# Optimization experiments

Measured on AMD Instinct MI355X. Metric: run time of the kernel, lower is better.

Reference implementation:

```python
import jax, jax.numpy as jnp
import numpy as np
from jax import lax

EPS = 1e-5  # torch BatchNorm2d default eps


def _binconv(x, w, b):
    # BinarizeConv2d: sign-binarize input and weight, dense conv, then add bias
    y = lax.conv_general_dilated(jnp.sign(x), jnp.sign(w), (2, 2), [(1, 1), (1, 1)],
                                 dimension_numbers=('NCHW', 'OIHW', 'NCHW'))
    return y + b[None, :, None, None]


def _bn(x, g, be):
    # BatchNorm2d in training mode: biased batch statistics over (N,H,W)
    m = jnp.mean(x, axis=(0, 2, 3), keepdims=True)
    v = jnp.mean((x - m) ** 2, axis=(0, 2, 3), keepdims=True)
    return (x - m) * (g[None, :, None, None] / jnp.sqrt(v + EPS)) + be[None, :, None, None]


def setup_inputs() -> dict:
    key = jax.random.key(0)
    ks = jax.random.split(key, 20)
    B = 8192
    d = {"x": jax.random.normal(ks[0], (B, 6, 32, 48), jnp.float32)}
    chans = [(12, 6), (24, 12), (48, 24), (96, 48)]
    i = 1
    for n, (co, ci) in enumerate(chans, 1):
        d[f"w{n}"] = jax.random.normal(ks[i], (co, ci, 5, 5), jnp.float32) * 0.1; i += 1
        d[f"b{n}"] = jax.random.normal(ks[i], (co,), jnp.float32) * 0.01; i += 1
        d[f"g{n}"] = jnp.ones((co,), jnp.float32)
        d[f"be{n}"] = jnp.zeros((co,), jnp.float32)
    d["wl"] = jax.random.normal(ks[i], (360, 192), jnp.float32) * 0.1; i += 1
    d["bl"] = jax.random.normal(ks[i], (360,), jnp.float32) * 0.01
    return d


def reference(x, w1, b1, g1, be1, w2, b2, g2, be2, w3, b3, g3, be3,
              w4, b4, g4, be4, wl, bl):
    x1 = jnp.clip(_bn(_binconv(x, w1, b1), g1, be1), 0.0, 1.0)
    x2 = jnp.clip(_bn(_binconv(x1, w2, b2), g2, be2), 0.0, 1.0)
    x3 = jnp.clip(_bn(_binconv(x2, w3, b3), g3, be3), 0.0, 1.0)
    x4 = jnp.clip(_bn(_binconv(x3, w4, b4), g4, be4), 0.0, 1.0)
    x4 = x4.reshape(-1, 192)  # (B, 96*1*2)
    # BinarizeLinear: in_features=192 != 784 so input is binarized too
    return jnp.sign(x4) @ jnp.sign(wl).T + bl
```

## Files before the change

### kernel.cpp

```cpp
#include <hip/hip_runtime.h>
#include <stdint.h>

typedef unsigned long long u64;
typedef uint32_t u32;
typedef uint16_t u16;

#define NIMG 8192

static const size_t O_TOT = 0;
static const size_t O_X1  = 4096;
static const size_t O_A2  = O_X1 + (size_t)NIMG*32*50*2;
static const size_t O_A3  = O_A2 + (size_t)NIMG*15*25*2;
static const size_t O_A4  = O_A3 + (size_t)NIMG*7*13*4;
static const size_t O_W1  = O_A4 + (size_t)NIMG*3*7*8;
static const size_t O_W2  = O_W1 + 120*8;
static const size_t O_W3  = O_W2 + 240*8;
static const size_t O_W4  = O_W3 + 960*8;
static const size_t O_WL  = O_W4 + 3840*8;
static const size_t O_S   = O_WL + 2160*8;

__global__ __launch_bounds__(256) void binx_k(const float* __restrict__ x,
                         const float* w1, const float* w2, const float* w3,
                         const float* w4, const float* wl,
                         u16* __restrict__ X1,
                         u64* W1, u64* W2, u64* W3, u64* W4, u64* WL, u64* tot) {
  if (blockIdx.x >= 49152) {
    int b = blockIdx.x - 49152;
    int t = threadIdx.x;
    if (b == 5) { tot[t] = 0; tot[t+256] = 0; return; }
    int u = b*256 + t;
    if (u < 60) {
      int co = u/5, kh = u%5;
      u64 wp=0, wn=0;
      for (int kw=0; kw<5; kw++) for (int ci=0; ci<6; ci++) {
        float v = w1[co*150 + ci*25 + kh*5 + kw];
        int pos = 6*kw + ci;
        if (v > 0.f) wp |= 1ull<<pos; else if (v < 0.f) wn |= 1ull<<pos;
      }
      W1[u*2]   = wp | (wn<<32);
      W1[u*2+1] = wn | (wp<<32);
    } else if (u < 180) {
      int q = u-60; int co=q/5, kh=q%5;
      u64 wp=0, wn=0;
      for (int kw=0; kw<5; kw++) for (int ci=0; ci<12; ci++) {
        float v = w2[co*300 + ci*25 + kh*5 + kw];
        int pos = 12*kw+ci;
        if (v>0.f) wp |= 1ull<<pos; else if (v<0.f) wn |= 1ull<<pos;
      }
      W2[q*2] = wp; W2[q*2+1] = wn;
    } else if (u < 420) {
      int q = u-180; int co=q/5, kh=q%5;
      u64 wp[2]={0,0}, wn[2]={0,0};
      for (int kw=0; kw<5; kw++) for (int ci=0; ci<24; ci++) {
        float v = w3[co*600 + ci*25 + kh*5 + kw];
        int pos = 24*kw+ci;
        if (v>0.f) wp[pos>>6] |= 1ull<<(pos&63); else if (v<0.f) wn[pos>>6] |= 1ull<<(pos&63);
      }
      W3[q*4]=wp[0]; W3[q*4+1]=wp[1]; W3[q*4+2]=wn[0]; W3[q*4+3]=wn[1];
    } else if (u < 900) {
      int q = u-420; int co=q/5, kh=q%5;
      u64 wp[4]={0,0,0,0}, wn[4]={0,0,0,0};
      for (int kw=0; kw<5; kw++) for (int ci=0; ci<48; ci++) {
        float v = w4[co*1200 + ci*25 + kh*5 + kw];
        int pos = 48*kw+ci;
        if (v>0.f) wp[pos>>6] |= 1ull<<(pos&63); else if (v<0.f) wn[pos>>6] |= 1ull<<(pos&63);
      }
      for (int j=0;j<4;j++){ W4[q*8+j]=wp[j]; W4[q*8+4+j]=wn[j]; }
    } else if (u < 1260) {
      int o = u-900;
      u64 wp[3]={0,0,0}, wn[3]={0,0,0};
      for (int k=0;k<192;k++){
        float v = wl[o*192+k];
        if (v>0.f) wp[k>>6] |= 1ull<<(k&63); else if (v<0.f) wn[k>>6] |= 1ull<<(k&63);
      }
      for (int j=0;j<3;j++){ WL[o*6+j]=wp[j]; WL[o*6+3+j]=wn[j]; }
    }
    return;
  }
  int gid = blockIdx.x*256+threadIdx.x;
  int n = gid / 1536, r = gid % 1536, h = r/48, w = r%48;
  const float* xp = x + (size_t)n*9216 + h*48 + w;
  u32 v = 0;
  #pragma unroll
  for (int c=0;c<6;c++){ float t = xp[c*1536];
    v |= (t>0.f ? 1u:0u)<<c; v |= (t<0.f ? 1u:0u)<<(8+c); }
  u16* row = X1 + (size_t)n*1600 + h*50;
  row[w+1] = (u16)v;
  if (w==0)  row[0]  = 0;
  if (w==47) row[49] = 0;
}

#define LSTR 265
template<int NR>
__device__ long long tree_reduce(const int (&vals)[NR], int* lds){
  int t = threadIdx.x;
  #pragma unroll
  for (int r=0;r<NR;r++) lds[r*LSTR + t] = vals[r];
  __syncthreads();
  if (t < NR*8) {
    int r = t % NR, seg = t / NR;
    const int* row = lds + r*LSTR + seg*32;
    int s = 0;
    #pragma unroll
    for (int i=0;i<32;i++) s += row[i];
    lds[r*LSTR + 256 + seg] = s;
  }
  __syncthreads();
  long long res = 0;
  if (t < NR) {
    const int* row = lds + t*LSTR + 256;
    int s = 0;
    #pragma unroll
    for (int i=0;i<8;i++) s += row[i];
    res = s;
  }
  __syncthreads();
  return res;
}

__global__ __launch_bounds__(256) void conv1_k(const u16* __restrict__ X1, const u64* __restrict__ W1,
                                               u32* __restrict__ S1) {
  int pix = blockIdx.x*256+threadIdx.x;
  int n = pix/345, r = pix%345, oh = r/23, ow = r%23;
  int S[12];
  #pragma unroll
  for (int i=0;i<12;i++) S[i]=0;
  const u16* base = X1 + (size_t)n*1600;
  for (int kh=0; kh<5; kh++){
    int row = 2*oh-1+kh;
    if ((unsigned)row >= 32u) continue;
    const u16* p = base + row*50 + 2*ow;
    u64 xp=0, xn=0;
    #pragma unroll
    for (int i=0;i<5;i++){ u32 v = p[i];
      xp |= (u64)(v & 63u) << (6*i);
      xn |= (u64)(v >> 8)  << (6*i); }
    u64 X = xp | (xn<<32);
    const u64* wr = W1 + kh*2;
    #pragma unroll
    for (int co=0;co<12;co++)
      S[co] += __popcll(X & wr[co*10]) - __popcll(X & wr[co*10+1]);
  }
  u32* o = S1 + (size_t)pix*3;
  #pragma unroll
  for (int j=0;j<3;j++)
    o[j] = (u32)(S[4*j]&255) | ((u32)(S[4*j+1]&255)<<8) |
           ((u32)(S[4*j+2]&255)<<16) | ((u32)(S[4*j+3]&255)<<24);
}

__global__ __launch_bounds__(256) void stats1_k(const u32* __restrict__ S1, u64* __restrict__ tot){
  __shared__ int lds[24*LSTR];
  int acc[12], q[12];
  #pragma unroll
  for (int i=0;i<12;i++){ acc[i]=0; q[i]=0; }
  int nt = gridDim.x*256;
  for (int p = blockIdx.x*256+threadIdx.x; p < NIMG*345; p += nt){
    u32 w0=S1[(size_t)p*3], w1=S1[(size_t)p*3+1], w2=S1[(size_t)p*3+2];
    #pragma unroll
    for (int c=0;c<12;c++){
      u32 w = (c<4)?w0:(c<8)?w1:w2;
      int v = (int)(w << ((3-(c&3))*8)) >> 24;
      acc[c]+=v; q[c]+=v*v;
    }
  }
  int vals[24];
  #pragma unroll
  for (int c=0;c<12;c++){ vals[c]=acc[c]; vals[12+c]=q[c]; }
  long long rs = tree_reduce<24>(vals, lds);
  int t = threadIdx.x;
  if (t < 12)       atomicAdd(&tot[t*2],        (u64)rs);
  else if (t < 24)  atomicAdd(&tot[(t-12)*2+1], (u64)rs);
}

__global__ __launch_bounds__(256) void conv2_k(const u16* __restrict__ A2, const u64* __restrict__ W2,
                                               short* __restrict__ S2, u64* __restrict__ tot) {
  __shared__ int lds[24*LSTR];
  int pix = blockIdx.x*256+threadIdx.x;
  int n = pix/77, r = pix%77, oh = r/11, ow = r%11;
  int S[24];
  #pragma unroll
  for (int i=0;i<24;i++) S[i]=0;
  const u16* base = A2 + (size_t)n*375;
  for (int kh=0; kh<5; kh++){
    int row = 2*oh-1+kh;
    if ((unsigned)row >= 15u) continue;
    const u16* p = base + row*25 + 2*ow;
    u64 X=0;
    #pragma unroll
    for (int i=0;i<5;i++) X |= (u64)p[i] << (12*i);
    const u64* wr = W2 + kh*2;
    #pragma unroll
    for (int co=0;co<24;co++)
      S[co] += __popcll(X & wr[co*10]) - __popcll(X & wr[co*10+1]);
  }
  short* o = S2 + (size_t)pix*24;
  #pragma unroll
  for (int co=0;co<24;co++) o[co] = (short)S[co];
  long long rs = tree_reduce<24>(S, lds);
  int t = threadIdx.x;
  if (t < 24) atomicAdd(&tot[t*2], (u64)rs);
  int q[24];
  #pragma unroll
  for (int c=0;c<24;c++) q[c]=S[c]*S[c];
  rs = tree_reduce<24>(q, lds);
  if (t < 24) atomicAdd(&tot[t*2+1], (u64)rs);
}

__global__ __launch_bounds__(256) void conv3_k(const u32* __restrict__ A3, const u64* __restrict__ W3,
                                               short* __restrict__ S3, u64* __restrict__ tot) {
  __shared__ int lds[24*LSTR];
  int pix = blockIdx.x*256+threadIdx.x;
  int n = pix/15, r = pix%15, oh = r/5, ow = r%5;
  int S[48];
  #pragma unroll
  for (int i=0;i<48;i++) S[i]=0;
  const u32* base = A3 + (size_t)n*91;
  for (int kh=0; kh<5; kh++){
    int row = 2*oh-1+kh;
    if ((unsigned)row >= 7u) continue;
    const u32* p = base + row*13 + 2*ow;
    u64 a0=p[0],a1=p[1],a2=p[2],a3=p[3],a4=p[4];
    u64 x0 = a0 | (a1<<24) | (a2<<48);
    u64 x1 = (a2>>16) | (a3<<8) | (a4<<32);
    const u64* wr = W3 + kh*4;
    #pragma unroll
    for (int co=0;co<48;co++){
      const u64* q = wr + co*20;
      S[co] += __popcll(x0 & q[0]) + __popcll(x1 & q[1])
             - __popcll(x0 & q[2]) - __popcll(x1 & q[3]);
    }
  }
  short* o = S3 + (size_t)pix*48;
  #pragma unroll
  for (int co=0;co<48;co++) o[co] = (short)S[co];
  int t = threadIdx.x;
  for (int c0=0; c0<48; c0+=24){
    int v[24];
    #pragma unroll
    for (int j=0;j<24;j++) v[j]=S[c0+j];
    long long rs = tree_reduce<24>(v, lds);
    if (t < 24) atomicAdd(&tot[(c0+t)*2], (u64)rs);
    #pragma unroll
    for (int j=0;j<24;j++) v[j]=S[c0+j]*S[c0+j];
    rs = tree_reduce<24>(v, lds);
    if (t < 24) atomicAdd(&tot[(c0+t)*2+1], (u64)rs);
  }
}

__global__ __launch_bounds__(256) void conv4_k(const u64* __restrict__ A4, const u64* __restrict__ W4,
                                               short* __restrict__ S4, u64* __restrict__ tot) {
  __shared__ int l4[96*66];
  int gid = blockIdx.x*256+threadIdx.x;
  int pix = gid>>2, grp = gid&3;
  int n = pix>>1, ow = pix&1;
  int S[24];
  #pragma unroll
  for (int i=0;i<24;i++) S[i]=0;
  const u64* base = A4 + (size_t)n*21;
  for (int kh=0; kh<5; kh++){
    int row = kh-1;
    if ((unsigned)row >= 3u) continue;
    const u64* p = base + row*7 + 2*ow;
    u64 a0=p[0],a1=p[1],a2=p[2],a3=p[3],a4=p[4];
    u64 x0 = a0 | (a1<<48);
    u64 x1 = (a1>>16) | (a2<<32);
    u64 x2 = (a2>>32) | (a3<<16);
    u64 x3 = a4;
    const u64* wr = W4 + kh*8;
    #pragma unroll
    for (int j=0;j<24;j++){
      const u64* q = wr + (grp*24+j)*40;
      S[j] += __popcll(x0&q[0]) + __popcll(x1&q[1]) + __popcll(x2&q[2]) + __popcll(x3&q[3])
            - __popcll(x0&q[4]) - __popcll(x1&q[5]) - __popcll(x2&q[6]) - __popcll(x3&q[7]);
    }
  }
  short* o = S4 + (size_t)pix*96 + grp*24;
  #pragma unroll
  for (int j=0;j<24;j++) o[j] = (short)S[j];
  int t = threadIdx.x, col = t>>2;
  #pragma unroll
  for (int j=0;j<24;j++) l4[(grp*24+j)*66 + col] = S[j];
  __syncthreads();
  if (t < 96){
    int s=0; const int* row = l4 + t*66;
    #pragma unroll
    for (int i=0;i<64;i++) s += row[i];
    atomicAdd(&tot[t*2], (u64)(long long)s);
  }
  __syncthreads();
  #pragma unroll
  for (int j=0;j<24;j++) l4[(grp*24+j)*66 + col] = S[j]*S[j];
  __syncthreads();
  if (t < 96){
    int s=0; const int* row = l4 + t*66;
    #pragma unroll
    for (int i=0;i<64;i++) s += row[i];
    atomicAdd(&tot[t*2+1], (u64)(long long)s);
  }
}

template<int C>
__device__ void bn_params(const u64* tot, const float* g, const float* be, double cnt,
                          float* s_mu, float* s_k, float* s_be) {
  int t = threadIdx.x;
  if (t < C) {
    long long sum = (long long)tot[t*2];
    long long sq  = (long long)tot[t*2+1];
    double mu  = (double)sum / cnt;
    double var = (double)sq / cnt - mu*mu;
    double kk  = (double)g[t] / sqrt(var + 1e-5);
    s_mu[t] = (float)mu; s_k[t] = (float)kk; s_be[t] = be[t];
  }
  __syncthreads();
}

__global__ __launch_bounds__(256) void thresh1_k(const u32* __restrict__ S1, const u64* tot,
                                                 const float* g, const float* be, u16* __restrict__ A2){
  __shared__ float mu[12], kk[12], bb[12];
  bn_params<12>(tot, g, be, 2826240.0, mu, kk, bb);
  int pix = blockIdx.x*256+threadIdx.x;
  int n=pix/345, r=pix%345, oh=r/23, ow=r%23;
  const u32* s = S1 + (size_t)pix*3;
  u32 w0=s[0], w1=s[1], w2=s[2];
  u32 wv=0;
  #pragma unroll
  for (int c=0;c<12;c++){
    u32 w = (c<4) ? w0 : (c<8) ? w1 : w2;
    int sv = (int)(w << ((3-(c&3))*8)) >> 24;
    float v = ((float)sv-mu[c])*kk[c]+bb[c];
    wv |= (v>0.f?1u:0u)<<c;
  }
  u16* row = A2 + (size_t)n*375 + oh*25;
  row[ow+1] = (u16)wv;
  if (ow==0)  row[0]  = 0;
  if (ow==22) row[24] = 0;
}

__global__ __launch_bounds__(256) void thresh2_k(const short* __restrict__ S2, const u64* tot,
                                                 const float* g, const float* be, u32* __restrict__ A3){
  __shared__ float mu[24], kk[24], bb[24];
  bn_params<24>(tot, g, be, 630784.0, mu, kk, bb);
  int pix = blockIdx.x*256+threadIdx.x;
  int n=pix/77, r=pix%77, oh=r/11, ow=r%11;
  const short* s = S2 + (size_t)pix*24;
  u32 wv=0;
  #pragma unroll
  for (int c=0;c<24;c++){ float v = ((float)s[c]-mu[c])*kk[c]+bb[c]; wv |= (v>0.f?1u:0u)<<c; }
  u32* row = A3 + (size_t)n*91 + oh*13;
  row[ow+1] = wv;
  if (ow==0)  row[0]  = 0;
  if (ow==10) row[12] = 0;
}

__global__ __launch_bounds__(256) void thresh3_k(const short* __restrict__ S3, const u64* tot,
                                                 const float* g, const float* be, u64* __restrict__ A4){
  __shared__ float mu[48], kk[48], bb[48];
  bn_params<48>(tot, g, be, 122880.0, mu, kk, bb);
  int pix = blockIdx.x*256+threadIdx.x;
  int n=pix/15, r=pix%15, oh=r/5, ow=r%5;
  const short* s = S3 + (size_t)pix*48;
  u64 wv=0;
  #pragma unroll
  for (int c=0;c<48;c++){ float v = ((float)s[c]-mu[c])*kk[c]+bb[c]; wv |= (u64)(v>0.f?1u:0u)<<c; }
  u64* row = A4 + (size_t)n*21 + oh*7;
  row[ow+1] = wv;
  if (ow==0) row[0] = 0;
  if (ow==4) row[6] = 0;
}

__global__ __launch_bounds__(256) void lin4_k(const short* __restrict__ S4, const u64* tot,
                                              const float* g, const float* be,
                                              const u64* __restrict__ WL, const float* __restrict__ bl,
                                              float* __restrict__ out){
  __shared__ float mu[96], kk[96], bb[96];
  __shared__ u64 aLs[64*3];
  __shared__ u64 wls[2160];
  bn_params<96>(tot, g, be, 16384.0, mu, kk, bb);
  int t = threadIdx.x;
  for (int i=t; i<2160; i+=256) wls[i] = WL[i];
  if (t < 64){
    int n = blockIdx.x*64 + t;
    u64 a[3]={0,0,0};
    for (int w=0;w<2;w++){
      const short* s = S4 + ((size_t)n*2+w)*96;
      #pragma unroll
      for (int c=0;c<96;c++){
        float v = ((float)s[c]-mu[c])*kk[c]+bb[c];
        int k = c*2+w;
        if (v>0.f) a[k>>6] |= 1ull<<(k&63);
      }
    }
    aLs[t*3]=a[0]; aLs[t*3+1]=a[1]; aLs[t*3+2]=a[2];
  }
  __syncthreads();
  float* ob = out + (size_t)blockIdx.x*23040;
  #pragma unroll 2
  for (int i=0;i<90;i++){
    int li = i*256+t;
    int nl = li/360, o = li%360;
    const u64* a = &aLs[nl*3];
    const u64* w = &wls[o*6];
    int S = __popcll(a[0]&w[0]) + __popcll(a[1]&w[1]) + __popcll(a[2]&w[2])
          - __popcll(a[0]&w[3]) - __popcll(a[1]&w[4]) - __popcll(a[2]&w[5]);
    ob[li] = (float)S + bl[o];
  }
}

extern "C" void kernel_launch(void* const* d_in, const int* in_sizes, int n_in,
                              void* d_out, int out_size, void* d_ws, size_t ws_size,
                              hipStream_t stream) {
  const float* x  = (const float*)d_in[0];
  const float* w1 = (const float*)d_in[1];
  const float* g1 = (const float*)d_in[3];
  const float* be1= (const float*)d_in[4];
  const float* w2 = (const float*)d_in[5];
  const float* g2 = (const float*)d_in[7];
  const float* be2= (const float*)d_in[8];
  const float* w3 = (const float*)d_in[9];
  const float* g3 = (const float*)d_in[11];
  const float* be3= (const float*)d_in[12];
  const float* w4 = (const float*)d_in[13];
  const float* g4 = (const float*)d_in[15];
  const float* be4= (const float*)d_in[16];
  const float* wl = (const float*)d_in[17];
  const float* bl = (const float*)d_in[18];

  char* ws = (char*)d_ws;
  u64* tot = (u64*)(ws + O_TOT);
  u16* X1  = (u16*)(ws + O_X1);
  u16* A2  = (u16*)(ws + O_A2);
  u32* A3  = (u32*)(ws + O_A3);
  u64* A4  = (u64*)(ws + O_A4);
  u64* W1  = (u64*)(ws + O_W1);
  u64* W2  = (u64*)(ws + O_W2);
  u64* W3  = (u64*)(ws + O_W3);
  u64* W4  = (u64*)(ws + O_W4);
  u64* WL  = (u64*)(ws + O_WL);
  u32*   S1b = (u32*)(ws + O_S);
  short* Sb  = (short*)(ws + O_S);

  binx_k<<<49158,256,0,stream>>>(x, w1,w2,w3,w4,wl, X1, W1,W2,W3,W4,WL, tot);

  conv1_k<<<11040,256,0,stream>>>(X1, W1, S1b);
  stats1_k<<<1024,256,0,stream>>>(S1b, tot+0);
  thresh1_k<<<11040,256,0,stream>>>(S1b, tot+0, g1, be1, A2);

  conv2_k<<<2464,256,0,stream>>>(A2, W2, Sb, tot+24);
  thresh2_k<<<2464,256,0,stream>>>(Sb, tot+24, g2, be2, A3);

  conv3_k<<<480,256,0,stream>>>(A3, W3, Sb, tot+72);
  thresh3_k<<<480,256,0,stream>>>(Sb, tot+72, g3, be3, A4);

  conv4_k<<<256,256,0,stream>>>(A4, W4, Sb, tot+168);
  lin4_k<<<128,256,0,stream>>>(Sb, tot+168, g4, be4, WL, bl, (float*)d_out);
}
```

Measured before the change: 882.2 us.

## Fuse input binarization into conv1 with per-image shared-memory bit image

Merges the input sign-binarization kernel and the first binary convolution into one kernel with one block per image. Each block loads its image with float4 reads, packs the sign bits into a shared-memory bitplane using atomicOr, and computes the W1 weight bits in shared memory. The conv1 popcount loop then reads that shared bitplane directly, so the X1 global intermediate and one launch go away. The costs are shared-memory atomics, 345 pixels spread over 256 threads (a second, mostly idle pass), and every block recomputing the W1 bits.

```diff
diff --git a/kernel.cpp b/kernel.cpp
--- a/kernel.cpp
+++ b/kernel.cpp
@@ -8,38 +8,26 @@
 #define NIMG 8192
 
 static const size_t O_TOT = 0;
-static const size_t O_X1  = 4096;
-static const size_t O_A2  = O_X1 + (size_t)NIMG*32*50*2;
+static const size_t O_A2  = 4096;
 static const size_t O_A3  = O_A2 + (size_t)NIMG*15*25*2;
 static const size_t O_A4  = O_A3 + (size_t)NIMG*7*13*4;
-static const size_t O_W1  = O_A4 + (size_t)NIMG*3*7*8;
-static const size_t O_W2  = O_W1 + 120*8;
+static const size_t O_W2  = O_A4 + (size_t)NIMG*3*7*8;
 static const size_t O_W3  = O_W2 + 240*8;
 static const size_t O_W4  = O_W3 + 960*8;
 static const size_t O_WL  = O_W4 + 3840*8;
 static const size_t O_S   = O_WL + 2160*8;
 
-__global__ __launch_bounds__(256) void binx_k(const float* __restrict__ x,
+__global__ __launch_bounds__(256) void bc1_k(const float* __restrict__ x,
                          const float* w1, const float* w2, const float* w3,
                          const float* w4, const float* wl,
-                         u16* __restrict__ X1,
-                         u64* W1, u64* W2, u64* W3, u64* W4, u64* WL, u64* tot) {
-  if (blockIdx.x >= 49152) {
-    int b = blockIdx.x - 49152;
+                         u64* W2, u64* W3, u64* W4, u64* WL, u64* tot,
+                         u32* __restrict__ S1) {
+  if (blockIdx.x >= NIMG) {
+    int b = blockIdx.x - NIMG;
     int t = threadIdx.x;
     if (b == 5) { tot[t] = 0; tot[t+256] = 0; return; }
     int u = b*256 + t;
-    if (u < 60) {
-      int co = u/5, kh = u%5;
-      u64 wp=0, wn=0;
-      for (int kw=0; kw<5; kw++) for (int ci=0; ci<6; ci++) {
-        float v = w1[co*150 + ci*25 + kh*5 + kw];
-        int pos = 6*kw + ci;
-        if (v > 0.f) wp |= 1ull<<pos; else if (v < 0.f) wn |= 1ull<<pos;
-      }
-      W1[u*2]   = wp | (wn<<32);
-      W1[u*2+1] = wn | (wp<<32);
-    } else if (u < 180) {
+    if (u >= 60 && u < 180) {
       int q = u-60; int co=q/5, kh=q%5;
       u64 wp=0, wn=0;
       for (int kw=0; kw<5; kw++) for (int ci=0; ci<12; ci++) {
@@ -48,7 +36,7 @@
         if (v>0.f) wp |= 1ull<<pos; else if (v<0.f) wn |= 1ull<<pos;
       }
       W2[q*2] = wp; W2[q*2+1] = wn;
-    } else if (u < 420) {
+    } else if (u >= 180 && u < 420) {
       int q = u-180; int co=q/5, kh=q%5;
       u64 wp[2]={0,0}, wn[2]={0,0};
       for (int kw=0; kw<5; kw++) for (int ci=0; ci<24; ci++) {
@@ -57,7 +45,7 @@
         if (v>0.f) wp[pos>>6] |= 1ull<<(pos&63); else if (v<0.f) wn[pos>>6] |= 1ull<<(pos&63);
       }
       W3[q*4]=wp[0]; W3[q*4+1]=wp[1]; W3[q*4+2]=wn[0]; W3[q*4+3]=wn[1];
-    } else if (u < 900) {
+    } else if (u >= 420 && u < 900) {
       int q = u-420; int co=q/5, kh=q%5;
       u64 wp[4]={0,0,0,0}, wn[4]={0,0,0,0};
       for (int kw=0; kw<5; kw++) for (int ci=0; ci<48; ci++) {
@@ -66,7 +54,7 @@
         if (v>0.f) wp[pos>>6] |= 1ull<<(pos&63); else if (v<0.f) wn[pos>>6] |= 1ull<<(pos&63);
       }
       for (int j=0;j<4;j++){ W4[q*8+j]=wp[j]; W4[q*8+4+j]=wn[j]; }
-    } else if (u < 1260) {
+    } else if (u >= 900 && u < 1260) {
       int o = u-900;
       u64 wp[3]={0,0,0}, wn[3]={0,0,0};
       for (int k=0;k<192;k++){
@@ -77,17 +65,71 @@
     }
     return;
   }
-  int gid = blockIdx.x*256+threadIdx.x;
-  int n = gid / 1536, r = gid % 1536, h = r/48, w = r%48;
-  const float* xp = x + (size_t)n*9216 + h*48 + w;
-  u32 v = 0;
-  #pragma unroll
-  for (int c=0;c<6;c++){ float t = xp[c*1536];
-    v |= (t>0.f ? 1u:0u)<<c; v |= (t<0.f ? 1u:0u)<<(8+c); }
-  u16* row = X1 + (size_t)n*1600 + h*50;
-  row[w+1] = (u16)v;
-  if (w==0)  row[0]  = 0;
-  if (w==47) row[49] = 0;
+
+  __shared__ u32 img[32*26];
+  __shared__ u64 W1s[120];
+  int t = threadIdx.x;
+  int n = blockIdx.x;
+
+  for (int i=t; i<832; i+=256) img[i] = 0;
+  if (t < 60) {
+    int co = t/5, kh = t%5;
+    u64 wp=0, wn=0;
+    for (int kw=0; kw<5; kw++) for (int ci=0; ci<6; ci++) {
+      float v = w1[co*150 + ci*25 + kh*5 + kw];
+      int pos = 6*kw + ci;
+      if (v > 0.f) wp |= 1ull<<pos; else if (v < 0.f) wn |= 1ull<<pos;
+    }
+    W1s[t*2]   = wp | (wn<<32);
+    W1s[t*2+1] = wn | (wp<<32);
+  }
+  __syncthreads();
+
+  const float4* xi = (const float4*)(x + (size_t)n*9216);
+  #pragma unroll
+  for (int k=0;k<9;k++){
+    int f = t + k*256;
+    int c = f/384, rr = f%384, h = rr/12, wg = rr%12;
+    float4 v = xi[f];
+    u32 b0 = ((v.x>0.f?1u:0u)<<c) | ((v.x<0.f?1u:0u)<<(8+c));
+    u32 b1 = ((v.y>0.f?1u:0u)<<c) | ((v.y<0.f?1u:0u)<<(8+c));
+    u32 b2 = ((v.z>0.f?1u:0u)<<c) | ((v.z<0.f?1u:0u)<<(8+c));
+    u32 b3 = ((v.w>0.f?1u:0u)<<c) | ((v.w<0.f?1u:0u)<<(8+c));
+    u32 wA = b0 | (b1<<16);
+    u32 wB = b2 | (b3<<16);
+    int base = h*26 + 2*wg + 1;
+    if (wA) atomicOr(&img[base],   wA);
+    if (wB) atomicOr(&img[base+1], wB);
+  }
+  __syncthreads();
+
+  for (int p = t; p < 345; p += 256){
+    int oh = p/23, ow = p%23;
+    int S[12];
+    #pragma unroll
+    for (int i=0;i<12;i++) S[i]=0;
+    for (int kh=0; kh<5; kh++){
+      int row = 2*oh-1+kh;
+      if ((unsigned)row >= 32u) continue;
+      const u32* wr3 = img + row*26 + ow;
+      u32 a=wr3[0], b=wr3[1], cc=wr3[2];
+      u32 p0=a>>16, p1=b&0xffffu, p2=b>>16, p3=cc&0xffffu, p4=cc>>16;
+      u64 xp = (u64)(p0&63u) | ((u64)(p1&63u)<<6) | ((u64)(p2&63u)<<12)
+             | ((u64)(p3&63u)<<18) | ((u64)(p4&63u)<<24);
+      u64 xn = (u64)(p0>>8) | ((u64)(p1>>8)<<6) | ((u64)(p2>>8)<<12)
+             | ((u64)(p3>>8)<<18) | ((u64)(p4>>8)<<24);
+      u64 X = xp | (xn<<32);
+      const u64* wr = W1s + kh*2;
+      #pragma unroll
+      for (int co=0;co<12;co++)
+        S[co] += __popcll(X & wr[co*10]) - __popcll(X & wr[co*10+1]);
+    }
+    u32* o = S1 + (size_t)(n*345+p)*3;
+    #pragma unroll
+    for (int j=0;j<3;j++)
+      o[j] = (u32)(S[4*j]&255) | ((u32)(S[4*j+1]&255)<<8) |
+             ((u32)(S[4*j+2]&255)<<16) | ((u32)(S[4*j+3]&255)<<24);
+  }
 }
 
 #define LSTR 265
@@ -116,36 +158,6 @@
   }
   __syncthreads();
   return res;
-}
-
-__global__ __launch_bounds__(256) void conv1_k(const u16* __restrict__ X1, const u64* __restrict__ W1,
-                                               u32* __restrict__ S1) {
-  int pix = blockIdx.x*256+threadIdx.x;
-  int n = pix/345, r = pix%345, oh = r/23, ow = r%23;
-  int S[12];
-  #pragma unroll
-  for (int i=0;i<12;i++) S[i]=0;
-  const u16* base = X1 + (size_t)n*1600;
-  for (int kh=0; kh<5; kh++){
-    int row = 2*oh-1+kh;
-    if ((unsigned)row >= 32u) continue;
-    const u16* p = base + row*50 + 2*ow;
-    u64 xp=0, xn=0;
-    #pragma unroll
-    for (int i=0;i<5;i++){ u32 v = p[i];
-      xp |= (u64)(v & 63u) << (6*i);
-      xn |= (u64)(v >> 8)  << (6*i); }
-    u64 X = xp | (xn<<32);
-    const u64* wr = W1 + kh*2;
-    #pragma unroll
-    for (int co=0;co<12;co++)
-      S[co] += __popcll(X & wr[co*10]) - __popcll(X & wr[co*10+1]);
-  }
-  u32* o = S1 + (size_t)pix*3;
-  #pragma unroll
-  for (int j=0;j<3;j++)
-    o[j] = (u32)(S[4*j]&255) | ((u32)(S[4*j+1]&255)<<8) |
-           ((u32)(S[4*j+2]&255)<<16) | ((u32)(S[4*j+3]&255)<<24);
 }
 
 __global__ __launch_bounds__(256) void stats1_k(const u32* __restrict__ S1, u64* __restrict__ tot){
@@ -427,11 +439,9 @@
 
   char* ws = (char*)d_ws;
   u64* tot = (u64*)(ws + O_TOT);
-  u16* X1  = (u16*)(ws + O_X1);
   u16* A2  = (u16*)(ws + O_A2);
   u32* A3  = (u32*)(ws + O_A3);
   u64* A4  = (u64*)(ws + O_A4);
-  u64* W1  = (u64*)(ws + O_W1);
   u64* W2  = (u64*)(ws + O_W2);
   u64* W3  = (u64*)(ws + O_W3);
   u64* W4  = (u64*)(ws + O_W4);
@@ -439,9 +449,7 @@
   u32*   S1b = (u32*)(ws + O_S);
   short* Sb  = (short*)(ws + O_S);
 
-  binx_k<<<49158,256,0,stream>>>(x, w1,w2,w3,w4,wl, X1, W1,W2,W3,W4,WL, tot);
-
-  conv1_k<<<11040,256,0,stream>>>(X1, W1, S1b);
+  bc1_k<<<NIMG+6,256,0,stream>>>(x, w1,w2,w3,w4,wl, W2,W3,W4,WL, tot, S1b);
   stats1_k<<<1024,256,0,stream>>>(S1b, tot+0);
   thresh1_k<<<11040,256,0,stream>>>(S1b, tot+0, g1, be1, A2);
 
```

Measured after the change: 1.128 ms. 27.9% more time.
